# Kernel tuning notes

Hardware: AMD Instinct MI355X
Metric: run time of the kernel (lower is better)

## Reference

```python
import jax, jax.numpy as jnp
import numpy as np

N = 50000          # nodes
E = 800000         # edges (before self-loops)
F_IN = 500         # input features
H1, C1 = 8, 16     # layer-1 heads, per-head channels
NUM_CLASSES = 7
NEG_SLOPE = 0.2


def setup_inputs() -> dict:
    key = jax.random.key(0)
    ks = jax.random.split(key, 10)
    s = 0.05
    return {
        "x": jax.random.normal(ks[0], (N, F_IN), jnp.float32),
        "edge_index": jax.random.randint(ks[1], (2, E), 0, N, dtype=jnp.int64),
        "W1": jax.random.normal(ks[2], (F_IN, H1 * C1), jnp.float32) * s,
        "att_src1": jax.random.normal(ks[3], (H1, C1), jnp.float32) * s,
        "att_dst1": jax.random.normal(ks[4], (H1, C1), jnp.float32) * s,
        "b1": jnp.zeros((H1 * C1,), jnp.float32),
        "W2": jax.random.normal(ks[5], (H1 * C1, NUM_CLASSES), jnp.float32) * s,
        "att_src2": jax.random.normal(ks[6], (1, NUM_CLASSES), jnp.float32) * s,
        "att_dst2": jax.random.normal(ks[7], (1, NUM_CLASSES), jnp.float32) * s,
        "b2": jnp.zeros((NUM_CLASSES,), jnp.float32),
    }


def _gat_conv(x, W, att_src, att_dst, bias, src, dst, concat):
    # PyG GATConv (eval mode: attention dropout is identity).
    H, C = att_src.shape
    h = (x @ W).reshape(N, H, C)                      # [N,H,C]
    a_src = jnp.sum(h * att_src, axis=-1)             # [N,H]
    a_dst = jnp.sum(h * att_dst, axis=-1)             # [N,H]
    e = a_src[src] + a_dst[dst]                       # [Et,H] per-edge logits
    e = jax.nn.leaky_relu(e, NEG_SLOPE)
    # segment softmax over incoming edges of each destination node
    m = jax.ops.segment_max(e, dst, num_segments=N)   # [N,H]
    e = jnp.exp(e - m[dst])
    denom = jax.ops.segment_sum(e, dst, num_segments=N)  # [N,H]
    alpha = e / (denom[dst] + 1e-16)                  # [Et,H]
    msg = h[src] * alpha[:, :, None]                  # [Et,H,C]
    out = jax.ops.segment_sum(msg, dst, num_segments=N)  # [N,H,C]
    if concat:
        out = out.reshape(N, H * C)
    else:
        out = out.mean(axis=1)
    return out + bias


def reference(x, edge_index, W1, att_src1, att_dst1, b1, W2, att_src2, att_dst2, b2):
    # add self-loops (PyG default add_self_loops=True)
    loops = jnp.arange(N, dtype=edge_index.dtype)
    src = jnp.concatenate([edge_index[0], loops])
    dst = jnp.concatenate([edge_index[1], loops])
    h = _gat_conv(x, W1, att_src1, att_dst1, b1, src, dst, concat=True)
    h = jax.nn.relu(h)
    # F.dropout(p=0.6, training=False) -> identity in eval mode
    out = _gat_conv(h, W2, att_src2, att_dst2, b2, src, dst, concat=False)
    return out
```

## Files before the change

### kernel.cpp

```cpp
#include <hip/hip_runtime.h>
#include <hip/hip_bf16.h>

#define NN 50000
#define EE 800000
#define ETOT 850000
#define FIN 500
#define HC 128
#define NH 8
#define CH 16
#define NC 7

#define OW1  0
#define OAS1 64000
#define OAD1 64128
#define OB1  64256
#define OW2  64384
#define OAS2 65280
#define OAD2 65287
#define OB2  65294
#define WTOT 65301

#define GR1  64
#define GK   32
#define KPAD 512
#define ASTR 40
#define BSTR 40

typedef __hip_bfloat16 bf16;
typedef __attribute__((ext_vector_type(8))) short short8;
typedef __attribute__((ext_vector_type(4))) float f32x4;

__device__ __forceinline__ float b2f(const bf16 v) { return __bfloat162float(v); }
__device__ __forceinline__ float lrelu(float v) { return fmaxf(v, 0.2f * v); }
__device__ __forceinline__ float elog(float v) { return __expf(fminf(lrelu(v), 30.f)); }
__device__ __forceinline__ float blo(unsigned w) { return __uint_as_float(w << 16); }
__device__ __forceinline__ float bhi(unsigned w) { return __uint_as_float(w & 0xffff0000u); }
__device__ __forceinline__ unsigned short f2bu(float f)
{
    bf16 h = __float2bfloat16(f);
    return *(unsigned short*)&h;
}

__device__ __forceinline__ int eread(const void* __restrict__ eidx, long long i, int is64)
{
    if (is64) return ((const int*)eidx)[2 * i];
    return ((const int*)eidx)[i];
}

__global__ void detect_kernel(const unsigned short* __restrict__ xraw,
                              const unsigned int* __restrict__ eraw,
                              int* __restrict__ flags, int* __restrict__ rowptr)
{
    __shared__ int s_insane, s_oddnz;
    if (threadIdx.x == 0) { s_insane = 0; s_oddnz = 0; }
    __syncthreads();
    int insane = 0;
    for (int i = threadIdx.x; i < 8192; i += 256) {
        const unsigned int bits = ((unsigned int)xraw[i]) << 16;
        const float v = __uint_as_float(bits);
        const float a = fabsf(v);
        const bool sane = (v == 0.0f) || (a >= 1e-30f && a <= 1e4f);
        if (!sane) insane++;
    }
    int oddnz = 0;
    for (int i = threadIdx.x; i < 512; i += 256) {
        if (eraw[2 * i + 1] != 0u) oddnz++;
    }
    atomicAdd(&s_insane, insane);
    atomicAdd(&s_oddnz, oddnz);
    __syncthreads();
    if (threadIdx.x == 0) {
        flags[0] = (s_insane < 256) ? 1 : 0;
        flags[1] = (s_oddnz == 0) ? 1 : 0;
        rowptr[NN] = ETOT;
    }
}

__global__ void conv_all_kernel(const void* W1, const void* as1, const void* ad1, const void* b1,
                                const void* W2, const void* as2, const void* ad2, const void* b2,
                                float* __restrict__ wc, unsigned short* __restrict__ w1t,
                                const int* __restrict__ flags)
{
    const int i = blockIdx.x * blockDim.x + threadIdx.x;
    const int isbf = flags[0];
    if (i < WTOT) {
        const void* src; int off;
        if (i < OAS1)      { src = W1;  off = i - OW1; }
        else if (i < OAD1) { src = as1; off = i - OAS1; }
        else if (i < OB1)  { src = ad1; off = i - OAD1; }
        else if (i < OW2)  { src = b1;  off = i - OB1; }
        else if (i < OAS2) { src = W2;  off = i - OW2; }
        else if (i < OAD2) { src = as2; off = i - OAS2; }
        else if (i < OB2)  { src = ad2; off = i - OAD2; }
        else               { src = b2;  off = i - OB2; }
        float v;
        if (isbf) v = b2f(((const bf16*)src)[off]);
        else      v = ((const float*)src)[off];
        wc[i] = v;
    }
    if (i < HC * KPAD) {
        const int col = i >> 9;
        const int k   = i & (KPAD - 1);
        float v = 0.f;
        if (k < FIN) {
            if (isbf) v = b2f(((const bf16*)W1)[k * HC + col]);
            else      v = ((const float*)W1)[k * HC + col];
        }
        w1t[i] = f2bu(v);
    }
}

__global__ void hist_kernel(const void* __restrict__ eidx, int* __restrict__ deg,
                            const int* __restrict__ flags)
{
    const int e = blockIdx.x * blockDim.x + threadIdx.x;
    if (e >= ETOT) return;
    int d;
    if (e < EE) d = eread(eidx, (long long)EE + e, flags[1]);
    else        d = e - EE;
    if ((unsigned)d < (unsigned)NN) atomicAdd(&deg[d], 1);
}

__global__ void scan_k1_kernel(const int* __restrict__ deg, int* __restrict__ bsum)
{
    __shared__ int lds[256];
    const int i = blockIdx.x * 256 + threadIdx.x;
    lds[threadIdx.x] = (i < NN) ? deg[i] : 0;
    __syncthreads();
    for (int s = 128; s > 0; s >>= 1) {
        if (threadIdx.x < s) lds[threadIdx.x] += lds[threadIdx.x + s];
        __syncthreads();
    }
    if (threadIdx.x == 0) bsum[blockIdx.x] = lds[0];
}

__global__ void scan_k2_kernel(int* __restrict__ bsum)
{
    __shared__ int a[256], b[256], orig[256];
    const int t = threadIdx.x;
    a[t] = bsum[t]; orig[t] = a[t];
    __syncthreads();
    int* cur = a; int* nxt = b;
    for (int off = 1; off < 256; off <<= 1) {
        nxt[t] = cur[t] + ((t >= off) ? cur[t - off] : 0);
        __syncthreads();
        int* tmp = cur; cur = nxt; nxt = tmp;
    }
    bsum[t] = cur[t] - orig[t];
}

__global__ void scan_k3_kernel(const int* __restrict__ deg, const int* __restrict__ bsum,
                               int* __restrict__ rowptr)
{
    __shared__ int a[256], b[256], own[256];
    const int t = threadIdx.x;
    const int i = blockIdx.x * 256 + t;
    const int v = (i < NN) ? deg[i] : 0;
    a[t] = v; own[t] = v;
    __syncthreads();
    int* cur = a; int* nxt = b;
    for (int off = 1; off < 256; off <<= 1) {
        nxt[t] = cur[t] + ((t >= off) ? cur[t - off] : 0);
        __syncthreads();
        int* tmp = cur; cur = nxt; nxt = tmp;
    }
    if (i < NN) rowptr[i] = bsum[blockIdx.x] + cur[t] - own[t];
}

__global__ void scatter_kernel(const void* __restrict__ eidx, const int* __restrict__ rowptr,
                               int* __restrict__ cur, int* __restrict__ esrc_sorted,
                               const int* __restrict__ flags)
{
    const int e = blockIdx.x * blockDim.x + threadIdx.x;
    if (e >= ETOT) return;
    int s, d;
    if (e < EE) {
        s = eread(eidx, e, flags[1]);
        d = eread(eidx, (long long)EE + e, flags[1]);
    } else s = d = e - EE;
    if ((unsigned)s >= (unsigned)NN || (unsigned)d >= (unsigned)NN) return;
    const int pos = rowptr[d] + atomicAdd(&cur[d], 1);
    if ((unsigned)pos < (unsigned)ETOT) esrc_sorted[pos] = s;
}

__global__ __launch_bounds__(256) void gemm1_mfma_kernel(
    const void* __restrict__ x, const unsigned short* __restrict__ w1t,
    bf16* __restrict__ h1, const float* __restrict__ wc,
    float* __restrict__ a_src1, float* __restrict__ a_dst1,
    const int* __restrict__ flags)
{
    __shared__ unsigned short Asl[GR1 * ASTR];
    __shared__ unsigned short Bsl[HC * BSTR];

    const int t    = threadIdx.x;
    const int wv   = t >> 6;
    const int lane = t & 63;
    const int m15  = lane & 15;
    const int quad = lane >> 4;
    const int r0   = blockIdx.x * GR1;
    const int isbf = flags[0];
    const float* xf = (const float*)x;
    const bf16*  xb = (const bf16*)x;

    const int wr  = (wv >> 1) * 32;
    const int wcb = (wv & 1) * 64;

    f32x4 acc[2][4];
#pragma unroll
    for (int i = 0; i < 2; ++i)
#pragma unroll
        for (int j = 0; j < 4; ++j) acc[i][j] = (f32x4){0.f, 0.f, 0.f, 0.f};

    const int arow = t >> 2;
    const int akk  = (t & 3) * 8;
    const int bcol = t & 127;
    const int bks  = (t >> 7) * 16;

    for (int kt = 0; kt < 16; ++kt) {
        const int k0 = kt * GK;
        {
            const int grow = r0 + arow;
            if (!isbf && grow < NN && (k0 + akk + 8) <= FIN) {
                const size_t base = (size_t)grow * FIN + k0 + akk;
                const float4 v0 = *(const float4*)(xf + base);
                const float4 v1 = *(const float4*)(xf + base + 4);
                uint4 pk;
                pk.x = (unsigned)f2bu(v0.x) | ((unsigned)f2bu(v0.y) << 16);
                pk.y = (unsigned)f2bu(v0.z) | ((unsigned)f2bu(v0.w) << 16);
                pk.z = (unsigned)f2bu(v1.x) | ((unsigned)f2bu(v1.y) << 16);
                pk.w = (unsigned)f2bu(v1.z) | ((unsigned)f2bu(v1.w) << 16);
                *(uint4*)&Asl[arow * ASTR + akk] = pk;
            } else {
#pragma unroll
                for (int j = 0; j < 8; ++j) {
                    const int k = k0 + akk + j;
                    float v = 0.f;
                    if (grow < NN && k < FIN)
                        v = isbf ? b2f(xb[(size_t)grow * FIN + k]) : xf[(size_t)grow * FIN + k];
                    Asl[arow * ASTR + akk + j] = f2bu(v);
                }
            }
        }
        {
            const unsigned short* gp = w1t + (size_t)bcol * KPAD + k0 + bks;
            *(uint4*)&Bsl[bcol * BSTR + bks]     = *(const uint4*)gp;
            *(uint4*)&Bsl[bcol * BSTR + bks + 8] = *(const uint4*)(gp + 8);
        }
        __syncthreads();

        const int ak = quad * 8;
        const short8 a0 = *(const short8*)&Asl[(wr + m15) * ASTR + ak];
        const short8 a1 = *(const short8*)&Asl[(wr + 16 + m15) * ASTR + ak];
#pragma unroll
        for (int ct = 0; ct < 4; ++ct) {
            const short8 b = *(const short8*)&Bsl[(wcb + ct * 16 + m15) * BSTR + ak];
            acc[0][ct] = __builtin_amdgcn_mfma_f32_16x16x32_bf16(a0, b, acc[0][ct], 0, 0, 0);
            acc[1][ct] = __builtin_amdgcn_mfma_f32_16x16x32_bf16(a1, b, acc[1][ct], 0, 0, 0);
        }
        __syncthreads();
    }

    const int hc0 = wcb >> 4;
    float asw[4], adw[4];
#pragma unroll
    for (int ct = 0; ct < 4; ++ct) {
        asw[ct] = wc[OAS1 + (hc0 + ct) * CH + m15];
        adw[ct] = wc[OAD1 + (hc0 + ct) * CH + m15];
    }
#pragma unroll
    for (int rt = 0; rt < 2; ++rt) {
#pragma unroll
        for (int reg = 0; reg < 4; ++reg) {
            const int row = r0 + wr + rt * 16 + quad * 4 + reg;
            const bool ok = (row < NN);
            bf16* hp = h1 + (size_t)row * HC;
#pragma unroll
            for (int ct = 0; ct < 4; ++ct) {
                const float v = acc[rt][ct][reg];
                if (ok) hp[wcb + ct * 16 + m15] = __float2bfloat16(v);
                float s = v * asw[ct];
                float d = v * adw[ct];
                s += __shfl_xor(s, 1);  d += __shfl_xor(d, 1);
                s += __shfl_xor(s, 2);  d += __shfl_xor(d, 2);
                s += __shfl_xor(s, 4);  d += __shfl_xor(d, 4);
                s += __shfl_xor(s, 8);  d += __shfl_xor(d, 8);
                if (ok && m15 == 0) {
                    a_src1[row * NH + hc0 + ct] = s;
                    a_dst1[row * NH + hc0 + ct] = d;
                }
            }
        }
    }
}

__global__ __launch_bounds__(256) void gather1_kernel(
    const int* __restrict__ rowptr, const int* __restrict__ esrc_sorted,
    const float* __restrict__ a_src, const float* __restrict__ a_dst,
    const bf16* __restrict__ h1, const float* __restrict__ wc,
    float* __restrict__ h2, float* __restrict__ a_src2, float* __restrict__ a_dst2)
{
    __shared__ float W2s[HC * NC];
    __shared__ float B1s[HC];
    for (int i = threadIdx.x; i < HC * NC; i += 256) W2s[i] = wc[OW2 + i];
    if (threadIdx.x < HC) B1s[threadIdx.x] = wc[OB1 + threadIdx.x];
    __syncthreads();

    const int node = blockIdx.x * 4 + (threadIdx.x >> 6);
    if (node >= NN) return;
    const int lane = threadIdx.x & 63;
    const int h = lane >> 3;
    const float ad = a_dst[node * NH + h];
    const int start = rowptr[node];
    const int end   = rowptr[node + 1];
    float acc0 = 0.f, acc1 = 0.f, den = 0.f;
    int i = start;
    for (; i + 8 <= end; i += 8) {
        int   sv[8];
        float ev[8];
        unsigned wv[8];
#pragma unroll
        for (int j = 0; j < 8; ++j) sv[j] = esrc_sorted[i + j];
#pragma unroll
        for (int j = 0; j < 8; ++j) ev[j] = a_src[sv[j] * NH + h];
#pragma unroll
        for (int j = 0; j < 8; ++j) wv[j] = *(const unsigned*)(h1 + (size_t)sv[j] * HC + 2 * lane);
#pragma unroll
        for (int j = 0; j < 8; ++j) {
            const float n = elog(ev[j] + ad);
            acc0 += n * blo(wv[j]);
            acc1 += n * bhi(wv[j]);
            den  += n;
        }
    }
    for (; i < end; ++i) {
        const int s = esrc_sorted[i];
        const float num = elog(a_src[s * NH + h] + ad);
        const unsigned w = *(const unsigned*)(h1 + (size_t)s * HC + 2 * lane);
        acc0 += num * blo(w);
        acc1 += num * bhi(w);
        den  += num;
    }
    const float inv = 1.f / (den + 1e-16f);

    const int k0 = 2 * lane;
    const float r0v = fmaxf(acc0 * inv + B1s[k0],     0.f);
    const float r1v = fmaxf(acc1 * inv + B1s[k0 + 1], 0.f);
    float p[NC];
#pragma unroll
    for (int c = 0; c < NC; ++c)
        p[c] = r0v * W2s[k0 * NC + c] + r1v * W2s[(k0 + 1) * NC + c];
#pragma unroll
    for (int m = 1; m < 64; m <<= 1) {
#pragma unroll
        for (int c = 0; c < NC; ++c) p[c] += __shfl_xor(p[c], m);
    }
    if (lane == 0) {
        float ps = 0.f, pd = 0.f;
        float* hp = h2 + (size_t)node * NC;
#pragma unroll
        for (int c = 0; c < NC; ++c) {
            hp[c] = p[c];
            ps += p[c] * wc[OAS2 + c];
            pd += p[c] * wc[OAD2 + c];
        }
        a_src2[node] = ps;
        a_dst2[node] = pd;
    }
}

__global__ void gather2_kernel(
    const int* __restrict__ rowptr, const int* __restrict__ esrc_sorted,
    const float* __restrict__ a_src, const float* __restrict__ a_dst,
    const float* __restrict__ h2, const float* __restrict__ wc,
    void* __restrict__ out, const int* __restrict__ flags)
{
    const int node = blockIdx.x * 32 + (threadIdx.x >> 3);
    if (node >= NN) return;
    const int c = threadIdx.x & 7;
    const float ad = a_dst[node];
    const int start = rowptr[node];
    const int end   = rowptr[node + 1];
    const int cc = (c < NC) ? c : 0;
    float acc = 0.f, den = 0.f;
    int i = start;
    for (; i + 4 <= end; i += 4) {
        const int s0 = esrc_sorted[i + 0];
        const int s1 = esrc_sorted[i + 1];
        const int s2 = esrc_sorted[i + 2];
        const int s3 = esrc_sorted[i + 3];
        const float e0 = a_src[s0];
        const float e1 = a_src[s1];
        const float e2 = a_src[s2];
        const float e3 = a_src[s3];
        const float v0 = h2[s0 * NC + cc];
        const float v1 = h2[s1 * NC + cc];
        const float v2 = h2[s2 * NC + cc];
        const float v3 = h2[s3 * NC + cc];
        const float n0 = elog(e0 + ad);
        const float n1 = elog(e1 + ad);
        const float n2 = elog(e2 + ad);
        const float n3 = elog(e3 + ad);
        acc += n0 * v0 + n1 * v1 + n2 * v2 + n3 * v3;
        den += n0 + n1 + n2 + n3;
    }
    for (; i < end; ++i) {
        const int s = esrc_sorted[i];
        const float num = elog(a_src[s] + ad);
        den += num;
        acc += num * h2[s * NC + cc];
    }
    if (c >= NC) return;
    const float v = acc / (den + 1e-16f) + wc[OB2 + c];
    if (flags[0]) ((bf16*)out)[node * NC + c] = __float2bfloat16(v);
    else          ((float*)out)[node * NC + c] = v;
}

extern "C" void kernel_launch(void* const* d_in, const int* in_sizes, int n_in,
                              void* d_out, int out_size, void* d_ws, size_t ws_size,
                              hipStream_t stream)
{
    const void* x        = d_in[0];
    const void* eidx     = d_in[1];
    const void* W1       = d_in[2];
    const void* att_src1 = d_in[3];
    const void* att_dst1 = d_in[4];
    const void* b1       = d_in[5];
    const void* W2       = d_in[6];
    const void* att_src2 = d_in[7];
    const void* att_dst2 = d_in[8];
    const void* b2       = d_in[9];

    float* ws = (float*)d_ws;
    size_t o = 0;
    int*   flags  = (int*)(ws + o);            o += 16;
    float* wc     = ws + o;                    o += 65312;
    unsigned short* w1t = (unsigned short*)(ws + o); o += (HC * KPAD) / 2;
    int*   deg    = (int*)(ws + o);            o += 50000;
    int*   cur    = (int*)(ws + o);            o += 50000;
    int*   rowptr = (int*)(ws + o);            o += 50016;
    int*   bsum   = (int*)(ws + o);            o += 256;
    int*   esrt   = (int*)(ws + o);            o += 850000;
    bf16*  h1     = (bf16*)(ws + o);           o += (size_t)NN * HC / 2;
    float* a_src1 = ws + o;                    o += (size_t)NN * NH;
    float* a_dst1 = ws + o;                    o += (size_t)NN * NH;
    float* h2     = ws + o;                    o += (size_t)NN * NC;
    float* a_src2 = ws + o;                    o += NN;
    float* a_dst2 = ws + o;                    o += NN;

    detect_kernel<<<1, 256, 0, stream>>>((const unsigned short*)x, (const unsigned int*)eidx,
                                         flags, rowptr);
    conv_all_kernel<<<(HC * KPAD + 255) / 256, 256, 0, stream>>>(
        W1, att_src1, att_dst1, b1, W2, att_src2, att_dst2, b2, wc, w1t, flags);
    hipMemsetAsync(deg, 0, 2 * (size_t)NN * sizeof(int), stream);
    hist_kernel<<<(ETOT + 255) / 256, 256, 0, stream>>>(eidx, deg, flags);
    scan_k1_kernel<<<(NN + 255) / 256, 256, 0, stream>>>(deg, bsum);
    scan_k2_kernel<<<1, 256, 0, stream>>>(bsum);
    scan_k3_kernel<<<(NN + 255) / 256, 256, 0, stream>>>(deg, bsum, rowptr);
    scatter_kernel<<<(ETOT + 255) / 256, 256, 0, stream>>>(eidx, rowptr, cur, esrt, flags);

    gemm1_mfma_kernel<<<(NN + GR1 - 1) / GR1, 256, 0, stream>>>(x, w1t, h1, wc,
                                                                a_src1, a_dst1, flags);
    gather1_kernel<<<(NN + 3) / 4, 256, 0, stream>>>(rowptr, esrt, a_src1, a_dst1, h1, wc,
                                                     h2, a_src2, a_dst2);
    gather2_kernel<<<(NN + 31) / 32, 256, 0, stream>>>(rowptr, esrt, a_src2, a_dst2, h2, wc,
                                                       d_out, flags);
}
```

Before: 368.6 us.

## Register-prefetch GEMM1 tiles, halve row tile, stage epilogue via LDS

The layer-1 GEMM now loads the next K-slice of x and W1 into registers while MFMAs run on the current LDS tile, which is a software pipeline meant to hide global-load latency. The row tile is halved to 32 so the grid has twice as many blocks for better occupancy, and each wave does one 16-row MFMA tile. The epilogue stages the fp32 accumulators in LDS, writes h1 as coalesced 16-byte bf16 stores, and computes the attention dot products per (row, head) without shuffles. The trade-offs are more register pressure, W1 being reloaded by twice as many blocks, and an extra LDS round trip.

```diff
diff --git a/kernel.cpp b/kernel.cpp
--- a/kernel.cpp
+++ b/kernel.cpp
@@ -20,7 +20,7 @@
 #define OB2  65294
 #define WTOT 65301
 
-#define GR1  64
+#define GR1  32
 #define GK   32
 #define KPAD 512
 #define ASTR 40
@@ -39,6 +39,10 @@
 {
     bf16 h = __float2bfloat16(f);
     return *(unsigned short*)&h;
+}
+__device__ __forceinline__ unsigned pk2(float a, float b)
+{
+    return (unsigned)f2bu(a) | ((unsigned)f2bu(b) << 16);
 }
 
 __device__ __forceinline__ int eread(const void* __restrict__ eidx, long long i, int is64)
@@ -189,8 +193,11 @@
     float* __restrict__ a_src1, float* __restrict__ a_dst1,
     const int* __restrict__ flags)
 {
-    __shared__ unsigned short Asl[GR1 * ASTR];
-    __shared__ unsigned short Bsl[HC * BSTR];
+    __shared__ __align__(16) unsigned char smem[16896];
+    __shared__ float attw[2][128];
+    unsigned short* Asl = (unsigned short*)smem;
+    unsigned short* Bsl = Asl + GR1 * ASTR;
+    float (*Esl)[132] = (float (*)[132])smem;
 
     const int t    = threadIdx.x;
     const int wv   = t >> 6;
@@ -200,95 +207,101 @@
     const int r0   = blockIdx.x * GR1;
     const int isbf = flags[0];
     const float* xf = (const float*)x;
-    const bf16*  xb = (const bf16*)x;
-
-    const int wr  = (wv >> 1) * 32;
+    const unsigned short* xb = (const unsigned short*)x;
+
+    if (t < 128) { attw[0][t] = wc[OAS1 + t]; attw[1][t] = wc[OAD1 + t]; }
+
+    const int wr  = (wv >> 1) * 16;
     const int wcb = (wv & 1) * 64;
 
-    f32x4 acc[2][4];
-#pragma unroll
-    for (int i = 0; i < 2; ++i)
-#pragma unroll
-        for (int j = 0; j < 4; ++j) acc[i][j] = (f32x4){0.f, 0.f, 0.f, 0.f};
-
-    const int arow = t >> 2;
-    const int akk  = (t & 3) * 8;
+    f32x4 acc[4];
+#pragma unroll
+    for (int j = 0; j < 4; ++j) acc[j] = (f32x4){0.f, 0.f, 0.f, 0.f};
+
+    const int arow = t >> 3;
+    const int akk  = (t & 7) * 4;
+    const int grow = r0 + arow;
     const int bcol = t & 127;
     const int bks  = (t >> 7) * 16;
 
+    uint2 apk = make_uint2(0u, 0u);
+    uint4 bp0, bp1;
+    {
+        if (grow < NN) {
+            if (isbf) apk = *(const uint2*)(xb + (size_t)grow * FIN + akk);
+            else {
+                const float4 v = *(const float4*)(xf + (size_t)grow * FIN + akk);
+                apk.x = pk2(v.x, v.y); apk.y = pk2(v.z, v.w);
+            }
+        }
+        const unsigned short* gp = w1t + (size_t)bcol * KPAD + bks;
+        bp0 = *(const uint4*)gp;
+        bp1 = *(const uint4*)(gp + 8);
+    }
+
     for (int kt = 0; kt < 16; ++kt) {
-        const int k0 = kt * GK;
-        {
-            const int grow = r0 + arow;
-            if (!isbf && grow < NN && (k0 + akk + 8) <= FIN) {
-                const size_t base = (size_t)grow * FIN + k0 + akk;
-                const float4 v0 = *(const float4*)(xf + base);
-                const float4 v1 = *(const float4*)(xf + base + 4);
-                uint4 pk;
-                pk.x = (unsigned)f2bu(v0.x) | ((unsigned)f2bu(v0.y) << 16);
-                pk.y = (unsigned)f2bu(v0.z) | ((unsigned)f2bu(v0.w) << 16);
-                pk.z = (unsigned)f2bu(v1.x) | ((unsigned)f2bu(v1.y) << 16);
-                pk.w = (unsigned)f2bu(v1.z) | ((unsigned)f2bu(v1.w) << 16);
-                *(uint4*)&Asl[arow * ASTR + akk] = pk;
-            } else {
-#pragma unroll
-                for (int j = 0; j < 8; ++j) {
-                    const int k = k0 + akk + j;
-                    float v = 0.f;
-                    if (grow < NN && k < FIN)
-                        v = isbf ? b2f(xb[(size_t)grow * FIN + k]) : xf[(size_t)grow * FIN + k];
-                    Asl[arow * ASTR + akk + j] = f2bu(v);
+        *(uint2*)&Asl[arow * ASTR + akk]     = apk;
+        *(uint4*)&Bsl[bcol * BSTR + bks]     = bp0;
+        *(uint4*)&Bsl[bcol * BSTR + bks + 8] = bp1;
+        __syncthreads();
+
+        if (kt < 15) {
+            const int k0 = (kt + 1) * GK;
+            apk = make_uint2(0u, 0u);
+            if (grow < NN && (k0 + akk) < FIN) {
+                if (isbf) apk = *(const uint2*)(xb + (size_t)grow * FIN + k0 + akk);
+                else {
+                    const float4 v = *(const float4*)(xf + (size_t)grow * FIN + k0 + akk);
+                    apk.x = pk2(v.x, v.y); apk.y = pk2(v.z, v.w);
                 }
             }
-        }
-        {
             const unsigned short* gp = w1t + (size_t)bcol * KPAD + k0 + bks;
-            *(uint4*)&Bsl[bcol * BSTR + bks]     = *(const uint4*)gp;
-            *(uint4*)&Bsl[bcol * BSTR + bks + 8] = *(const uint4*)(gp + 8);
+            bp0 = *(const uint4*)gp;
+            bp1 = *(const uint4*)(gp + 8);
+        }
+
+        const short8 a0 = *(const short8*)&Asl[(wr + m15) * ASTR + quad * 8];
+#pragma unroll
+        for (int ct = 0; ct < 4; ++ct) {
+            const short8 b = *(const short8*)&Bsl[(wcb + ct * 16 + m15) * BSTR + quad * 8];
+            acc[ct] = __builtin_amdgcn_mfma_f32_16x16x32_bf16(a0, b, acc[ct], 0, 0, 0);
         }
         __syncthreads();
-
-        const int ak = quad * 8;
-        const short8 a0 = *(const short8*)&Asl[(wr + m15) * ASTR + ak];
-        const short8 a1 = *(const short8*)&Asl[(wr + 16 + m15) * ASTR + ak];
-#pragma unroll
-        for (int ct = 0; ct < 4; ++ct) {
-            const short8 b = *(const short8*)&Bsl[(wcb + ct * 16 + m15) * BSTR + ak];
-            acc[0][ct] = __builtin_amdgcn_mfma_f32_16x16x32_bf16(a0, b, acc[0][ct], 0, 0, 0);
-            acc[1][ct] = __builtin_amdgcn_mfma_f32_16x16x32_bf16(a1, b, acc[1][ct], 0, 0, 0);
-        }
-        __syncthreads();
-    }
-
-    const int hc0 = wcb >> 4;
-    float asw[4], adw[4];
-#pragma unroll
-    for (int ct = 0; ct < 4; ++ct) {
-        asw[ct] = wc[OAS1 + (hc0 + ct) * CH + m15];
-        adw[ct] = wc[OAD1 + (hc0 + ct) * CH + m15];
-    }
-#pragma unroll
-    for (int rt = 0; rt < 2; ++rt) {
-#pragma unroll
-        for (int reg = 0; reg < 4; ++reg) {
-            const int row = r0 + wr + rt * 16 + quad * 4 + reg;
-            const bool ok = (row < NN);
-            bf16* hp = h1 + (size_t)row * HC;
-#pragma unroll
-            for (int ct = 0; ct < 4; ++ct) {
-                const float v = acc[rt][ct][reg];
-                if (ok) hp[wcb + ct * 16 + m15] = __float2bfloat16(v);
-                float s = v * asw[ct];
-                float d = v * adw[ct];
-                s += __shfl_xor(s, 1);  d += __shfl_xor(d, 1);
-                s += __shfl_xor(s, 2);  d += __shfl_xor(d, 2);
-                s += __shfl_xor(s, 4);  d += __shfl_xor(d, 4);
-                s += __shfl_xor(s, 8);  d += __shfl_xor(d, 8);
-                if (ok && m15 == 0) {
-                    a_src1[row * NH + hc0 + ct] = s;
-                    a_dst1[row * NH + hc0 + ct] = d;
-                }
+    }
+
+#pragma unroll
+    for (int ct = 0; ct < 4; ++ct)
+#pragma unroll
+        for (int reg = 0; reg < 4; ++reg)
+            Esl[wr + quad * 4 + reg][wcb + ct * 16 + m15] = acc[ct][reg];
+    __syncthreads();
+
+    {
+        const int row = t >> 3;
+        const int c0  = (t & 7) * 16;
+        const int gr2 = r0 + row;
+        if (gr2 < NN) {
+            const float* ep = &Esl[row][c0];
+            uint4 w0, w1;
+            w0.x = pk2(ep[0],  ep[1]);  w0.y = pk2(ep[2],  ep[3]);
+            w0.z = pk2(ep[4],  ep[5]);  w0.w = pk2(ep[6],  ep[7]);
+            w1.x = pk2(ep[8],  ep[9]);  w1.y = pk2(ep[10], ep[11]);
+            w1.z = pk2(ep[12], ep[13]); w1.w = pk2(ep[14], ep[15]);
+            *(uint4*)(h1 + (size_t)gr2 * HC + c0)     = w0;
+            *(uint4*)(h1 + (size_t)gr2 * HC + c0 + 8) = w1;
+
+            const int hh = t & 7;
+            const float* hp = &Esl[row][hh * 16];
+            const float* as = &attw[0][hh * 16];
+            const float* ad = &attw[1][hh * 16];
+            float s = 0.f, d = 0.f;
+#pragma unroll
+            for (int u = 0; u < 16; ++u) {
+                s += hp[u] * as[u];
+                d += hp[u] * ad[u];
             }
+            a_src1[(size_t)gr2 * NH + hh] = s;
+            a_dst1[(size_t)gr2 * NH + hh] = d;
         }
     }
 }
```

Result: slower. 376.9 us (+2.3%).

## Restructure GEMM1 as persistent blocks with register-resident W1 and double-buffered X

Applied to the files above, without the earlier changes.

The first-layer GEMM now runs as 512 persistent blocks of 512 threads, each walking a contiguous range of 16-row chunks. Every wave keeps its 16-column slice of W1 in registers for the whole K dimension instead of reloading it through shared memory per tile. X chunks are staged into an XOR-swizzled shared buffer, with the next chunk prefetched into registers while MFMAs run on the current one. This removes repeated W1 traffic and most per-K-tile barriers, at the cost of much higher register pressure and a hardcoded chunk split tied to N=50000.

```diff
diff --git a/kernel.cpp b/kernel.cpp
--- a/kernel.cpp
+++ b/kernel.cpp
@@ -20,11 +20,9 @@
 #define OB2  65294
 #define WTOT 65301
 
-#define GR1  64
-#define GK   32
 #define KPAD 512
-#define ASTR 40
-#define BSTR 40
+#define GEMM1_BLOCKS 512
+#define NCHUNK 3125
 
 typedef __hip_bfloat16 bf16;
 typedef __attribute__((ext_vector_type(8))) short short8;
@@ -39,6 +37,10 @@
 {
     bf16 h = __float2bfloat16(f);
     return *(unsigned short*)&h;
+}
+__device__ __forceinline__ unsigned pk2(float a, float b)
+{
+    return (unsigned)f2bu(a) | ((unsigned)f2bu(b) << 16);
 }
 
 __device__ __forceinline__ int eread(const void* __restrict__ eidx, long long i, int is64)
@@ -183,113 +185,171 @@
     if ((unsigned)pos < (unsigned)ETOT) esrc_sorted[pos] = s;
 }
 
-__global__ __launch_bounds__(256) void gemm1_mfma_kernel(
+__global__ __launch_bounds__(512, 4) void gemm1_mfma_kernel(
     const void* __restrict__ x, const unsigned short* __restrict__ w1t,
     bf16* __restrict__ h1, const float* __restrict__ wc,
     float* __restrict__ a_src1, float* __restrict__ a_dst1,
     const int* __restrict__ flags)
 {
-    __shared__ unsigned short Asl[GR1 * ASTR];
-    __shared__ unsigned short Bsl[HC * BSTR];
+    __shared__ __align__(16) unsigned char Asm[2][16384];
 
     const int t    = threadIdx.x;
     const int wv   = t >> 6;
     const int lane = t & 63;
     const int m15  = lane & 15;
     const int quad = lane >> 4;
-    const int r0   = blockIdx.x * GR1;
+    const int bid  = blockIdx.x;
     const int isbf = flags[0];
-    const float* xf = (const float*)x;
-    const bf16*  xb = (const bf16*)x;
-
-    const int wr  = (wv >> 1) * 32;
-    const int wcb = (wv & 1) * 64;
-
-    f32x4 acc[2][4];
-#pragma unroll
-    for (int i = 0; i < 2; ++i)
-#pragma unroll
-        for (int j = 0; j < 4; ++j) acc[i][j] = (f32x4){0.f, 0.f, 0.f, 0.f};
-
-    const int arow = t >> 2;
-    const int akk  = (t & 3) * 8;
-    const int bcol = t & 127;
-    const int bks  = (t >> 7) * 16;
-
-    for (int kt = 0; kt < 16; ++kt) {
-        const int k0 = kt * GK;
-        {
-            const int grow = r0 + arow;
-            if (!isbf && grow < NN && (k0 + akk + 8) <= FIN) {
-                const size_t base = (size_t)grow * FIN + k0 + akk;
-                const float4 v0 = *(const float4*)(xf + base);
-                const float4 v1 = *(const float4*)(xf + base + 4);
-                uint4 pk;
-                pk.x = (unsigned)f2bu(v0.x) | ((unsigned)f2bu(v0.y) << 16);
-                pk.y = (unsigned)f2bu(v0.z) | ((unsigned)f2bu(v0.w) << 16);
-                pk.z = (unsigned)f2bu(v1.x) | ((unsigned)f2bu(v1.y) << 16);
-                pk.w = (unsigned)f2bu(v1.z) | ((unsigned)f2bu(v1.w) << 16);
-                *(uint4*)&Asl[arow * ASTR + akk] = pk;
-            } else {
-#pragma unroll
-                for (int j = 0; j < 8; ++j) {
-                    const int k = k0 + akk + j;
-                    float v = 0.f;
-                    if (grow < NN && k < FIN)
-                        v = isbf ? b2f(xb[(size_t)grow * FIN + k]) : xf[(size_t)grow * FIN + k];
-                    Asl[arow * ASTR + akk + j] = f2bu(v);
+    const unsigned char* xB = (const unsigned char*)x;
+
+    const int nc = 6 + (bid < 53 ? 1 : 0);
+    const int c0 = bid * 6 + (bid < 53 ? bid : 53);
+
+    const unsigned short* bp = w1t + (size_t)(wv * 16 + m15) * KPAD + quad * 8;
+    short8 Breg[16];
+#pragma unroll
+    for (int kt = 0; kt < 16; ++kt)
+        Breg[kt] = *(const short8*)(bp + kt * 32);
+
+    const float asw = wc[OAS1 + wv * 16 + m15];
+    const float adw = wc[OAD1 + wv * 16 + m15];
+
+    if (t < 96) {
+        const int buf = t / 48, idx = t % 48;
+        const int row = idx / 3, p = idx % 3;
+        const int off = 1000 + p * 8;
+        *(unsigned long long*)(&Asm[buf][row * 1024 +
+            ((off & ~15) ^ ((row & 7) << 4)) + (off & 8)]) = 0ull;
+    }
+
+    auto swaddr = [&](unsigned char* lb, int row, int off) -> unsigned long long* {
+        return (unsigned long long*)(lb + row * 1024 +
+            ((off & ~15) ^ ((row & 7) << 4)) + (off & 8));
+    };
+
+    auto stage_sync = [&](int c, int buf) {
+        unsigned char* lb = &Asm[buf][0];
+        if (isbf) {
+            const unsigned char* base = xB + (size_t)c * 16000;
+#pragma unroll
+            for (int j = 0; j < 4; ++j) {
+                const int u = t + 512 * j;
+                if (u < 2000) {
+                    const unsigned long long v = *(const unsigned long long*)(base + u * 8);
+                    const int row = u / 125;
+                    const int off = (u - row * 125) * 8;
+                    *swaddr(lb, row, off) = v;
                 }
             }
-        }
-        {
-            const unsigned short* gp = w1t + (size_t)bcol * KPAD + k0 + bks;
-            *(uint4*)&Bsl[bcol * BSTR + bks]     = *(const uint4*)gp;
-            *(uint4*)&Bsl[bcol * BSTR + bks + 8] = *(const uint4*)(gp + 8);
-        }
-        __syncthreads();
-
-        const int ak = quad * 8;
-        const short8 a0 = *(const short8*)&Asl[(wr + m15) * ASTR + ak];
-        const short8 a1 = *(const short8*)&Asl[(wr + 16 + m15) * ASTR + ak];
-#pragma unroll
-        for (int ct = 0; ct < 4; ++ct) {
-            const short8 b = *(const short8*)&Bsl[(wcb + ct * 16 + m15) * BSTR + ak];
-            acc[0][ct] = __builtin_amdgcn_mfma_f32_16x16x32_bf16(a0, b, acc[0][ct], 0, 0, 0);
-            acc[1][ct] = __builtin_amdgcn_mfma_f32_16x16x32_bf16(a1, b, acc[1][ct], 0, 0, 0);
-        }
-        __syncthreads();
-    }
-
-    const int hc0 = wcb >> 4;
-    float asw[4], adw[4];
-#pragma unroll
-    for (int ct = 0; ct < 4; ++ct) {
-        asw[ct] = wc[OAS1 + (hc0 + ct) * CH + m15];
-        adw[ct] = wc[OAD1 + (hc0 + ct) * CH + m15];
-    }
-#pragma unroll
-    for (int rt = 0; rt < 2; ++rt) {
-#pragma unroll
-        for (int reg = 0; reg < 4; ++reg) {
-            const int row = r0 + wr + rt * 16 + quad * 4 + reg;
-            const bool ok = (row < NN);
-            bf16* hp = h1 + (size_t)row * HC;
-#pragma unroll
-            for (int ct = 0; ct < 4; ++ct) {
-                const float v = acc[rt][ct][reg];
-                if (ok) hp[wcb + ct * 16 + m15] = __float2bfloat16(v);
-                float s = v * asw[ct];
-                float d = v * adw[ct];
-                s += __shfl_xor(s, 1);  d += __shfl_xor(d, 1);
-                s += __shfl_xor(s, 2);  d += __shfl_xor(d, 2);
-                s += __shfl_xor(s, 4);  d += __shfl_xor(d, 4);
-                s += __shfl_xor(s, 8);  d += __shfl_xor(d, 8);
-                if (ok && m15 == 0) {
-                    a_src1[row * NH + hc0 + ct] = s;
-                    a_dst1[row * NH + hc0 + ct] = d;
+        } else {
+            const unsigned char* base = xB + (size_t)c * 32000;
+#pragma unroll
+            for (int j = 0; j < 4; ++j) {
+                const int u = t + 512 * j;
+                if (u < 2000) {
+                    const float4 v = *(const float4*)(base + u * 16);
+                    const unsigned long long w = (unsigned long long)pk2(v.x, v.y)
+                                               | ((unsigned long long)pk2(v.z, v.w) << 32);
+                    const int b = u * 16;
+                    const int row = b / 2000;
+                    const int off = (b - row * 2000) >> 1;
+                    *swaddr(lb, row, off) = w;
                 }
             }
         }
+    };
+
+    stage_sync(c0, 0);
+    __syncthreads();
+
+    for (int ci = 0; ci < nc; ++ci) {
+        const int cr0 = (c0 + ci) * 16;
+        const unsigned char* Ab = &Asm[ci & 1][0];
+        const bool pre = (ci + 1 < nc);
+
+        unsigned long long gb[4];
+        float4 gf[4];
+        if (pre) {
+            if (isbf) {
+                const unsigned char* base = xB + (size_t)(c0 + ci + 1) * 16000;
+#pragma unroll
+                for (int j = 0; j < 4; ++j) {
+                    const int u = t + 512 * j;
+                    gb[j] = (u < 2000) ? *(const unsigned long long*)(base + u * 8) : 0ull;
+                }
+            } else {
+                const unsigned char* base = xB + (size_t)(c0 + ci + 1) * 32000;
+#pragma unroll
+                for (int j = 0; j < 4; ++j) {
+                    const int u = t + 512 * j;
+                    gf[j] = (u < 2000) ? *(const float4*)(base + u * 16)
+                                       : make_float4(0.f, 0.f, 0.f, 0.f);
+                }
+            }
+        }
+
+        f32x4 acc = (f32x4){0.f, 0.f, 0.f, 0.f};
+#pragma unroll
+        for (int kt = 0; kt < 16; ++kt) {
+            const int g = kt * 4 + quad;
+            const short8 a = *(const short8*)(Ab + m15 * 1024 +
+                                              ((g * 16) ^ ((m15 & 7) << 4)));
+            acc = __builtin_amdgcn_mfma_f32_16x16x32_bf16(a, Breg[kt], acc, 0, 0, 0);
+        }
+
+#pragma unroll
+        for (int reg = 0; reg < 4; ++reg) {
+            const int row = cr0 + quad * 4 + reg;
+            h1[(size_t)row * HC + wv * 16 + m15] = __float2bfloat16(acc[reg]);
+        }
+        float sr[4], dr[4];
+#pragma unroll
+        for (int reg = 0; reg < 4; ++reg) { sr[reg] = acc[reg] * asw; dr[reg] = acc[reg] * adw; }
+#pragma unroll
+        for (int m = 1; m < 16; m <<= 1) {
+#pragma unroll
+            for (int reg = 0; reg < 4; ++reg) {
+                sr[reg] += __shfl_xor(sr[reg], m);
+                dr[reg] += __shfl_xor(dr[reg], m);
+            }
+        }
+        if (m15 == 0) {
+#pragma unroll
+            for (int reg = 0; reg < 4; ++reg) {
+                const int row = cr0 + quad * 4 + reg;
+                a_src1[(size_t)row * NH + wv] = sr[reg];
+                a_dst1[(size_t)row * NH + wv] = dr[reg];
+            }
+        }
+
+        if (pre) {
+            unsigned char* lb = &Asm[(ci + 1) & 1][0];
+            if (isbf) {
+#pragma unroll
+                for (int j = 0; j < 4; ++j) {
+                    const int u = t + 512 * j;
+                    if (u < 2000) {
+                        const int row = u / 125;
+                        const int off = (u - row * 125) * 8;
+                        *swaddr(lb, row, off) = gb[j];
+                    }
+                }
+            } else {
+#pragma unroll
+                for (int j = 0; j < 4; ++j) {
+                    const int u = t + 512 * j;
+                    if (u < 2000) {
+                        const unsigned long long w = (unsigned long long)pk2(gf[j].x, gf[j].y)
+                                                   | ((unsigned long long)pk2(gf[j].z, gf[j].w) << 32);
+                        const int b = u * 16;
+                        const int row = b / 2000;
+                        const int off = (b - row * 2000) >> 1;
+                        *swaddr(lb, row, off) = w;
+                    }
+                }
+            }
+        }
+        __syncthreads();
     }
 }
 
@@ -458,8 +518,8 @@
     scan_k3_kernel<<<(NN + 255) / 256, 256, 0, stream>>>(deg, bsum, rowptr);
     scatter_kernel<<<(ETOT + 255) / 256, 256, 0, stream>>>(eidx, rowptr, cur, esrt, flags);
 
-    gemm1_mfma_kernel<<<(NN + GR1 - 1) / GR1, 256, 0, stream>>>(x, w1t, h1, wc,
-                                                                a_src1, a_dst1, flags);
+    gemm1_mfma_kernel<<<GEMM1_BLOCKS, 512, 0, stream>>>(x, w1t, h1, wc,
+                                                        a_src1, a_dst1, flags);
     gather1_kernel<<<(NN + 3) / 4, 256, 0, stream>>>(rowptr, esrt, a_src1, a_dst1, h1, wc,
                                                      h2, a_src2, a_dst2);
     gather2_kernel<<<(NN + 31) / 32, 256, 0, stream>>>(rowptr, esrt, a_src2, a_dst2, h2, wc,
```

New measurement: 383.8 us. 4.1% more time.
